# Optimization experiments

Measured on AMD Instinct MI355X. Metric: run time of the kernel, lower is better.

Reference implementation:

```python
import jax, jax.numpy as jnp
import numpy as np

K = 3  # number of nearest neighbors
EPS = 1e-10


def setup_inputs() -> dict:
    key = jax.random.key(0)
    k1, k2, k3 = jax.random.split(key, 3)
    B, C, N = 2, 3, 8192
    xyz1 = jax.random.normal(k1, (B, C, N), dtype=jnp.float32)
    xyz2 = jax.random.normal(k2, (B, C, N), dtype=jnp.float32)
    flow1 = jax.random.normal(k3, (B, C, N), dtype=jnp.float32) * 0.1
    return {"xyz1": xyz1, "xyz2": xyz2, "flow1": flow1}


def _square_distance(src, dst):
    # src: [B, N, 3], dst: [B, M, 3] -> [B, N, M]
    d = -2.0 * jnp.einsum('bnc,bmc->bnm', src, dst)
    d = d + jnp.sum(src ** 2, axis=-1)[:, :, None]
    d = d + jnp.sum(dst ** 2, axis=-1)[:, None, :]
    return d


def _gather_group(points, idx):
    # points: [B, N, C], idx: [B, S, K] -> [B, S, K, C]
    return jax.vmap(lambda p, i: p[i])(points, idx)


def reference(xyz1, xyz2, flow1):
    B, C, N1 = xyz1.shape
    N2 = xyz2.shape[2]
    xyz1_to_2 = (xyz1 + flow1).transpose(0, 2, 1)  # [B, N1, 3]
    xyz2_t = xyz2.transpose(0, 2, 1)               # [B, N2, 3]
    flow1_t = flow1.transpose(0, 2, 1)             # [B, N1, 3]

    sqrdists = _square_distance(xyz2_t, xyz1_to_2)  # [B, N2, N1]
    _, knn_idx = jax.lax.top_k(-sqrdists, K)        # smallest K -> [B, N2, K]

    grouped_xyz = _gather_group(xyz1_to_2, knn_idx)           # [B, N2, K, 3]
    diff = grouped_xyz - xyz2_t[:, :, None, :]                 # [B, N2, K, 3]
    dist = jnp.maximum(jnp.linalg.norm(diff, axis=3), EPS)     # [B, N2, K]
    inv = 1.0 / dist
    weight = inv / jnp.sum(inv, axis=2, keepdims=True)         # [B, N2, K]

    grouped_flow = _gather_group(flow1_t, knn_idx)             # [B, N2, K, 3]
    flow2 = jnp.sum(weight[..., None] * grouped_flow, axis=2)  # [B, N2, 3]
    warped_xyz2 = (xyz2_t - flow2).transpose(0, 2, 1)          # [B, 3, N2]
    return warped_xyz2
```

## Files before the change

### kernel.cpp

```cpp
#include <hip/hip_runtime.h>


#define NPTS   8192
#define BLOCK  256
#define Q      4
#define QPB    8
#define HALF   4096
#define KMASK  0xFFFFFF80
#define EPSV   1e-10f

__device__ __forceinline__ float rfl_f32(float x) {
    return __int_as_float(__builtin_amdgcn_readfirstlane(__float_as_int(x)));
}

__device__ __forceinline__ void ksort3(float k, float& m0, float& m1, float& m2) {
    m2 = __builtin_amdgcn_fmed3f(k, m1, m2);
    m1 = __builtin_amdgcn_fmed3f(k, m0, m1);
    m0 = fminf(k, m0);
}

__device__ __forceinline__ float pack_key(float d, int jg, int km) {
    int r;
    asm("v_and_or_b32 %0, %1, %2, %3"
        : "=v"(r)
        : "v"(__float_as_int(d)), "s"(km), "v"(jg));
    return __int_as_float(r);
}

__device__ __forceinline__ void insert3_idx(float k, int idx,
                                            float& m0, float& m1, float& m2,
                                            int& j0, int& j1, int& j2) {
    const bool c0 = k < m0;
    const bool c1 = k < m1;
    const bool c2 = k < m2;
    ksort3(k, m0, m1, m2);
    j2 = c1 ? j1 : (c2 ? idx : j2);
    j1 = c0 ? j0 : (c1 ? idx : j1);
    j0 = c0 ? idx : j0;
}

__global__ __launch_bounds__(256)
void warp_points_kernel(const float* __restrict__ xyz1,
                        const float* __restrict__ flow1,
                        float4* __restrict__ ws, int total) {
    const int i = blockIdx.x * 256 + threadIdx.x;
    if (i >= total) return;
    const int b = i / NPTS, n = i - b * NPTS;
    const float* x1 = xyz1 + (size_t)b * 3 * NPTS;
    const float* f1 = flow1 + (size_t)b * 3 * NPTS;
    const float px = x1[0*NPTS + n] + f1[0*NPTS + n];
    const float py = x1[1*NPTS + n] + f1[1*NPTS + n];
    const float pz = x1[2*NPTS + n] + f1[2*NPTS + n];
    ws[i] = make_float4(px, py, pz, 0.0f);
}

#define BODY(P, JG)                                                    \
    {                                                                  \
        _Pragma("unroll")                                              \
        for (int i = 0; i < Q; ++i) {                                  \
            const float dx = (P).x - qx[i];                            \
            const float dy = (P).y - qy[i];                            \
            const float dz = (P).z - qz[i];                            \
            const float d  = fmaf(dx, dx, fmaf(dy, dy, dz * dz));      \
            const float kk = pack_key(d, (JG), km);                    \
            ksort3(kk, k0[i], k1[i], k2[i]);                           \
        }                                                              \
    }

__global__ __launch_bounds__(BLOCK, 8)
void pointwarp_kernel(const float4* __restrict__ wsp,
                      const float* __restrict__ xyz2,
                      const float* __restrict__ flow1,
                      float* __restrict__ out) {
    __shared__ float s_k[2][2][Q][3];
    __shared__ int   s_i[2][2][Q][3];

    const int tid  = threadIdx.x;
    const int w    = tid >> 6;
    const int t    = tid & 63;
    const int pair = w >> 1;
    const int w2   = w & 1;
    const int blocksPerB = NPTS / QPB;
    const int b     = blockIdx.x / blocksPerB;
    const int qblk  = (blockIdx.x % blocksPerB) * QPB;
    const int qbase = qblk + pair * Q;

    const float4* cand = wsp + (size_t)b * NPTS;
    const float*  x2   = xyz2 + (size_t)b * 3 * NPTS;
    const float*  f1   = flow1 + (size_t)b * 3 * NPTS;

    float qx[Q], qy[Q], qz[Q], k0[Q], k1[Q], k2[Q];
    #pragma unroll
    for (int i = 0; i < Q; ++i) {
        qx[i] = rfl_f32(x2[0*NPTS + qbase + i]);
        qy[i] = rfl_f32(x2[1*NPTS + qbase + i]);
        qz[i] = rfl_f32(x2[2*NPTS + qbase + i]);
        k0[i] = k1[i] = k2[i] = 3e38f;
    }

    const float4* base = cand + w2 * HALF + t;
    const int km = KMASK;
    int jga = w2 * (HALF / 64);
    float4 c0 = base[0];
    float4 c1 = base[64];
    float4 c2 = base[128];
    float4 c3 = base[192];
    #pragma unroll 2
    for (int j = 0; j < HALF / 128 - 2; ++j) {
        const float4 n0 = base[(j + 2) * 128];
        const float4 n1 = base[(j + 2) * 128 + 64];
        BODY(c0, jga)
        BODY(c1, jga + 1)
        c0 = c2; c1 = c3; c2 = n0; c3 = n1;
        jga += 2;
    }
    BODY(c0, jga)
    BODY(c1, jga + 1)
    BODY(c2, jga + 2)
    BODY(c3, jga + 3)

    float a0[Q], a1[Q], a2[Q];
    #pragma unroll
    for (int i = 0; i < Q; ++i) { a0[i] = k0[i]; a1[i] = k1[i]; a2[i] = k2[i]; }

    #pragma unroll
    for (int step = 1; step < 64; step <<= 1) {
        #pragma unroll
        for (int i = 0; i < Q; ++i) {
            const float b0 = __shfl_xor(k0[i], step, 64);
            const float b1 = __shfl_xor(k1[i], step, 64);
            const float b2 = __shfl_xor(k2[i], step, 64);
            ksort3(b0, k0[i], k1[i], k2[i]);
            ksort3(b1, k0[i], k1[i], k2[i]);
            ksort3(b2, k0[i], k1[i], k2[i]);
        }
    }

    int i0[Q], i1[Q], i2[Q];
    #pragma unroll
    for (int i = 0; i < Q; ++i) {
        {
            const float kf = k0[i];
            const unsigned long long m = __ballot(kf == a0[i] || kf == a1[i] || kf == a2[i]);
            i0[i] = ((__float_as_int(kf) & 0x7F) << 6) | (__ffsll(m) - 1);
        }
        {
            const float kf = k1[i];
            const unsigned long long m = __ballot(kf == a0[i] || kf == a1[i] || kf == a2[i]);
            i1[i] = ((__float_as_int(kf) & 0x7F) << 6) | (__ffsll(m) - 1);
        }
        {
            const float kf = k2[i];
            const unsigned long long m = __ballot(kf == a0[i] || kf == a1[i] || kf == a2[i]);
            i2[i] = ((__float_as_int(kf) & 0x7F) << 6) | (__ffsll(m) - 1);
        }
    }

    #pragma unroll
    for (int i = 0; i < Q; ++i) {
        if (t == i) {
            s_k[pair][w2][i][0] = k0[i]; s_i[pair][w2][i][0] = i0[i];
            s_k[pair][w2][i][1] = k1[i]; s_i[pair][w2][i][1] = i1[i];
            s_k[pair][w2][i][2] = k2[i]; s_i[pair][w2][i][2] = i2[i];
        }
    }
    __syncthreads();

    if (tid < QPB) {
        const int u  = tid;
        const int pr = u >> 2, qi = u & 3;
        float m0 = 3e38f, m1 = 3e38f, m2 = 3e38f;
        int   j0 = 0, j1 = 0, j2 = 0;
        #pragma unroll
        for (int wv = 0; wv < 2; ++wv) {
            #pragma unroll
            for (int s = 0; s < 3; ++s) {
                insert3_idx(s_k[pr][wv][qi][s], s_i[pr][wv][qi][s],
                            m0, m1, m2, j0, j1, j2);
            }
        }
        const int n2 = qblk + u;
        const float gx = x2[0*NPTS + n2];
        const float gy = x2[1*NPTS + n2];
        const float gz = x2[2*NPTS + n2];
        float dd[3];
        const int js[3] = {j0, j1, j2};
        #pragma unroll
        for (int s = 0; s < 3; ++s) {
            const float4 p = cand[js[s]];
            const float dx = p.x - gx, dy = p.y - gy, dz = p.z - gz;
            dd[s] = fmaf(dx, dx, fmaf(dy, dy, dz*dz));
        }
        float w0 = 1.0f / fmaxf(sqrtf(dd[0]), EPSV);
        float w1 = 1.0f / fmaxf(sqrtf(dd[1]), EPSV);
        float w2v = 1.0f / fmaxf(sqrtf(dd[2]), EPSV);
        const float ws = w0 + w1 + w2v;
        w0 /= ws; w1 /= ws; w2v /= ws;

        float* o = out + (size_t)b * 3 * NPTS;
        #pragma unroll
        for (int c = 0; c < 3; ++c) {
            const float fl = w0  * f1[c*NPTS + j0]
                           + w1  * f1[c*NPTS + j1]
                           + w2v * f1[c*NPTS + j2];
            o[c*NPTS + n2] = x2[c*NPTS + n2] - fl;
        }
    }
}

extern "C" void kernel_launch(void* const* d_in, const int* in_sizes, int n_in,
                              void* d_out, int out_size, void* d_ws, size_t ws_size,
                              hipStream_t stream) {
    const float* xyz1  = (const float*)d_in[0];
    const float* xyz2  = (const float*)d_in[1];
    const float* flow1 = (const float*)d_in[2];
    float* out = (float*)d_out;
    float4* ws = (float4*)d_ws;

    const int B = in_sizes[0] / (3 * NPTS);
    const int total = B * NPTS;
    warp_points_kernel<<<(total + 255) / 256, 256, 0, stream>>>(xyz1, flow1, ws, total);
    const int grid = B * (NPTS / QPB);
    pointwarp_kernel<<<grid, BLOCK, 0, stream>>>(ws, xyz2, flow1, out);
}
```

Baseline: 99.12 us.

## Hand-schedule candidate loads with inline asm 4-stage prefetch ring

```diff
diff --git a/kernel.cpp b/kernel.cpp
--- a/kernel.cpp
+++ b/kernel.cpp
@@ -8,6 +8,8 @@
 #define HALF   4096
 #define KMASK  0xFFFFFF80
 #define EPSV   1e-10f
+
+typedef float f32x4 __attribute__((ext_vector_type(4)));
 
 __device__ __forceinline__ float rfl_f32(float x) {
     return __int_as_float(__builtin_amdgcn_readfirstlane(__float_as_int(x)));
@@ -58,16 +60,28 @@
     {                                                                  \
         _Pragma("unroll")                                              \
         for (int i = 0; i < Q; ++i) {                                  \
-            const float dx = (P).x - qx[i];                            \
-            const float dy = (P).y - qy[i];                            \
-            const float dz = (P).z - qz[i];                            \
+            const float dx = (P)[0] - qx[i];                           \
+            const float dy = (P)[1] - qy[i];                           \
+            const float dz = (P)[2] - qz[i];                           \
             const float d  = fmaf(dx, dx, fmaf(dy, dy, dz * dz));      \
             const float kk = pack_key(d, (JG), km);                    \
             ksort3(kk, k0[i], k1[i], k2[i]);                           \
         }                                                              \
     }
 
-__global__ __launch_bounds__(BLOCK, 8)
+#define ISSUE(B0, B1)                                                  \
+    do {                                                               \
+        asm volatile("global_load_dwordx4 %0, %2, %3\n\t"              \
+                     "global_load_dwordx4 %1, %2, %3 offset:1024"      \
+                     : "=&v"(B0), "=&v"(B1)                            \
+                     : "v"(vo), "s"(cand));                            \
+        vo += 2048u;                                                   \
+    } while (0)
+
+#define WAITC(N, B0, B1)                                               \
+    asm volatile("s_waitcnt vmcnt(" #N ")" : "+v"(B0), "+v"(B1))
+
+__global__ __launch_bounds__(BLOCK, 4)
 void pointwarp_kernel(const float4* __restrict__ wsp,
                       const float* __restrict__ xyz2,
                       const float* __restrict__ flow1,
@@ -98,26 +112,41 @@
         k0[i] = k1[i] = k2[i] = 3e38f;
     }
 
-    const float4* base = cand + w2 * HALF + t;
     const int km = KMASK;
+    uint32_t vo = (uint32_t)(w2 * (HALF * 16)) + (uint32_t)t * 16u;
     int jga = w2 * (HALF / 64);
-    float4 c0 = base[0];
-    float4 c1 = base[64];
-    float4 c2 = base[128];
-    float4 c3 = base[192];
-    #pragma unroll 2
-    for (int j = 0; j < HALF / 128 - 2; ++j) {
-        const float4 n0 = base[(j + 2) * 128];
-        const float4 n1 = base[(j + 2) * 128 + 64];
-        BODY(c0, jga)
-        BODY(c1, jga + 1)
-        c0 = c2; c1 = c3; c2 = n0; c3 = n1;
-        jga += 2;
-    }
-    BODY(c0, jga)
-    BODY(c1, jga + 1)
-    BODY(c2, jga + 2)
-    BODY(c3, jga + 3)
+
+    f32x4 e0, e1, fa0, fa1, g0, g1, h0, h1;
+
+    asm volatile("s_waitcnt vmcnt(0)" ::: "memory");
+
+    ISSUE(e0, e1);
+    ISSUE(fa0, fa1);
+    ISSUE(g0, g1);
+    ISSUE(h0, h1);
+
+    for (int jj = 0; jj < 7; ++jj) {
+        WAITC(6, e0, e1);
+        BODY(e0, jga) BODY(e1, jga + 1) jga += 2;
+        ISSUE(e0, e1);
+        WAITC(6, fa0, fa1);
+        BODY(fa0, jga) BODY(fa1, jga + 1) jga += 2;
+        ISSUE(fa0, fa1);
+        WAITC(6, g0, g1);
+        BODY(g0, jga) BODY(g1, jga + 1) jga += 2;
+        ISSUE(g0, g1);
+        WAITC(6, h0, h1);
+        BODY(h0, jga) BODY(h1, jga + 1) jga += 2;
+        ISSUE(h0, h1);
+    }
+    WAITC(6, e0, e1);
+    BODY(e0, jga) BODY(e1, jga + 1) jga += 2;
+    WAITC(4, fa0, fa1);
+    BODY(fa0, jga) BODY(fa1, jga + 1) jga += 2;
+    WAITC(2, g0, g1);
+    BODY(g0, jga) BODY(g1, jga + 1) jga += 2;
+    WAITC(0, h0, h1);
+    BODY(h0, jga) BODY(h1, jga + 1) jga += 2;
 
     float a0[Q], a1[Q], a2[Q];
     #pragma unroll
```

New measurement: 97.78 us. No clear change (-1.4%).
